# Kernel optimization log

Measured on AMD Instinct MI355X. Metric: run time of the kernel, lower is better.

The kernel has to match this reference:

```python
import jax, jax.numpy as jnp
import numpy as np

H = 128          # hidden / embed dim
NH = 4           # attention heads
HD = H // NH     # head dim = 32
MFD = 4          # missile feat dim
FOD = 15         # full obs dim
NEG_SLOPE = 0.01 # LeakyReLU default


def _gru(x_seq, h0, wih, whh, bih, bhh):
    # x_seq: [B,S,H], h0: [B,H]; torch GRU gate math
    def step(h, x):
        gi = x @ wih.T + bih            # [B,3H]
        gh = h @ whh.T + bhh
        i_r, i_z, i_n = jnp.split(gi, 3, axis=-1)
        h_r, h_z, h_n = jnp.split(gh, 3, axis=-1)
        r = jax.nn.sigmoid(i_r + h_r)
        z = jax.nn.sigmoid(i_z + h_z)
        n = jnp.tanh(i_n + r * h_n)
        h_new = (1.0 - z) * n + z * h
        return h_new, h_new
    h_last, outs = jax.lax.scan(step, h0, jnp.swapaxes(x_seq, 0, 1))
    return jnp.swapaxes(outs, 0, 1), h_last  # [B,S,H], [B,H]


def _ln(x, w, b, eps=1e-5):
    mu = jnp.mean(x, axis=-1, keepdims=True)
    var = jnp.var(x, axis=-1, keepdims=True)
    return (x - mu) * jax.lax.rsqrt(var + eps) * w + b


def setup_inputs() -> dict:
    key = jax.random.key(0)
    ks = jax.random.split(key, 24)
    B, S = 4096, 64
    s = 0.02
    p = {
        "obs": jax.random.normal(ks[0], (B, S, FOD), jnp.float32),
        "h0": jnp.zeros((1, B, H), jnp.float32),
        "enc_air_w": jax.random.normal(ks[1], (H, FOD)) * s,
        "enc_air_b": jnp.zeros((H,)),
        "enc_m_w": jax.random.normal(ks[2], (H, MFD)) * s,
        "enc_m_b": jnp.zeros((H,)),
        "gru_wih": jax.random.normal(ks[3], (3 * H, H)) * s,
        "gru_whh": jax.random.normal(ks[4], (3 * H, H)) * s,
        "gru_bih": jnp.zeros((3 * H,)),
        "gru_bhh": jnp.zeros((3 * H,)),
        "qln_w": jnp.ones((H,)), "qln_b": jnp.zeros((H,)),
        "kln_w": jnp.ones((H,)), "kln_b": jnp.zeros((H,)),
        "attn_in_w": jax.random.normal(ks[5], (3 * H, H)) * s,
        "attn_in_b": jnp.zeros((3 * H,)),
        "attn_out_w": jax.random.normal(ks[6], (H, H)) * s,
        "attn_out_b": jnp.zeros((H,)),
        "mlp0_w": jax.random.normal(ks[7], (H, H)) * s,
        "mlp0_b": jnp.zeros((H,)),
        "mlp1_w": jax.random.normal(ks[8], (H, H)) * s,
        "mlp1_b": jnp.zeros((H,)),
        "fco_w": jax.random.normal(ks[9], (1, H)) * s,
        "fco_b": jnp.zeros((1,)),
    }
    return {k: v.astype(jnp.float32) for k, v in p.items()}


def reference(obs, h0, enc_air_w, enc_air_b, enc_m_w, enc_m_b,
              gru_wih, gru_whh, gru_bih, gru_bhh,
              qln_w, qln_b, kln_w, kln_b,
              attn_in_w, attn_in_b, attn_out_w, attn_out_b,
              mlp0_w, mlp0_b, mlp1_w, mlp1_b, fco_w, fco_b):
    B, S, _ = obs.shape
    N = B * S
    # aircraft encoder + GRU with residual
    air_embed = obs @ enc_air_w.T + enc_air_b                      # [B,S,H]
    gru_out, h_last = _gru(air_embed, h0[0], gru_wih, gru_whh, gru_bih, gru_bhh)
    air_feat = (gru_out + air_embed).reshape(N, H)                 # [N,H]
    # missile encoders (shared weights, two missiles)
    m_raw = obs[..., :2 * MFD].reshape(N, 2, MFD)                  # [N,2,4]
    keys_raw = m_raw @ enc_m_w.T + enc_m_b                         # [N,2,H]
    # inactive-missile mask
    inactive = jnp.array([1.0, 0.0, 1.0, 0.0], obs.dtype)
    mask = jnp.all(jnp.isclose(m_raw, inactive, rtol=1e-5, atol=1e-8), axis=-1)  # [N,2]
    # layer norms
    q_n = _ln(air_feat[:, None, :], qln_w, qln_b)                  # [N,1,H]
    k_n = _ln(keys_raw, kln_w, kln_b)                              # [N,2,H]
    # multihead attention (1 query, 2 keys), values are raw keys
    wq, wk, wv = jnp.split(attn_in_w, 3, axis=0)
    bq, bk, bv = jnp.split(attn_in_b, 3, axis=0)
    q = (q_n @ wq.T + bq).reshape(N, 1, NH, HD)
    k = (k_n @ wk.T + bk).reshape(N, 2, NH, HD)
    v = (keys_raw @ wv.T + bv).reshape(N, 2, NH, HD)
    scores = jnp.einsum('nqhd,nkhd->nhqk', q, k) / jnp.sqrt(jnp.float32(HD))
    scores = scores + jnp.where(mask, -jnp.inf, 0.0)[:, None, None, :]
    attn = jax.nn.softmax(scores, axis=-1)                         # [N,NH,1,2]
    ctx = jnp.einsum('nhqk,nkhd->nqhd', attn, v).reshape(N, H)
    attn_out = ctx @ attn_out_w.T + attn_out_b                     # [N,H]
    attn_out = jnp.where(jnp.isnan(attn_out), 0.0, attn_out)       # nan_to_num guard
    combined = air_feat + attn_out
    # MLP head
    h1 = jax.nn.leaky_relu(combined @ mlp0_w.T + mlp0_b, NEG_SLOPE)
    h2 = jax.nn.leaky_relu(h1 @ mlp1_w.T + mlp1_b, NEG_SLOPE)
    val = h2 @ fco_w.T + fco_b                                     # [N,1]
    return val, h_last[None]
```

## Files before the change

kernel.cpp:

```cpp
#include <hip/hip_runtime.h>
#include <math.h>

#define B_   4096
#define S_   64
#define H_   128
#define N_   (B_*S_)

#define WS_WC    0
#define WS_BC    6144
#define WS_WAP   6528
#define WS_WQP   8576
#define WS_SQ    24960
#define WS_EQ    25088
#define WS_KC    25216
#define WS_EK1   25728
#define WS_SK    25856
#define WS_EK2   25984
#define WS_VC    26112
#define WS_VB    26624
#define WS_MV    26752
#define WS_QQ    26756
#define WS_QLIN  26772
#define WS_MBC   26776
#define WS_C0    26777
#define WS_PB    27392
#define WS_WO2T  (WS_PB + 5120)
#define WS_SROW  (WS_PB + 7808)
#define WS_EROW  (WS_PB + 7836)
#define WS_GB    60160
#define WS_AIR   92928
#define TOKS     64

typedef __attribute__((ext_vector_type(8))) short bf16x8;
typedef __attribute__((ext_vector_type(4))) float f32x4;

extern "C" __device__ float __ocml_native_exp2_f32(float);

__device__ __forceinline__ float dot4(float4 a, float4 b){
    return fmaf(a.x,b.x, fmaf(a.y,b.y, fmaf(a.z,b.z, a.w*b.w)));
}
__device__ __forceinline__ unsigned short f2bf(float f){
    union { float f; unsigned u; } v; v.f = f;
    unsigned r = v.u + 0x7FFF + ((v.u >> 16) & 1);
    return (unsigned short)(r >> 16);
}
__device__ __forceinline__ float bf2f(unsigned short u){
    union { unsigned u; float f; } v; v.u = ((unsigned)u) << 16;
    return v.f;
}
__device__ __forceinline__ unsigned cvtpk_bf16(float a, float b){
    unsigned r;
    asm("v_cvt_pk_bf16_f32 %0, %1, %2" : "=v"(r) : "v"(a), "v"(b));
    return r;
}

#define KL_SCALE (-1.4426950408889634f)
#define KN_SCALE ( 2.8853900817779268f)

__global__ void precompute_kernel(
    const float* __restrict__ enc_air_w, const float* __restrict__ enc_air_b,
    const float* __restrict__ enc_m_w,  const float* __restrict__ enc_m_b,
    const float* __restrict__ gru_wih,  const float* __restrict__ gru_bih,
    const float* __restrict__ qln_w, const float* __restrict__ qln_b,
    const float* __restrict__ kln_w, const float* __restrict__ kln_b,
    const float* __restrict__ attn_in_w, const float* __restrict__ attn_in_b,
    const float* __restrict__ attn_out_w,
    const float* __restrict__ mlp0_w, const float* __restrict__ mlp1_w,
    float* __restrict__ ws)
{
    int i = blockIdx.x*blockDim.x + threadIdx.x;
    if (i < 6144) {
        int o = i>>4, f = i&15; float a = 0.f;
        if (f < 15) for (int k=0;k<128;k++) a = fmaf(gru_wih[o*128+k], enc_air_w[k*15+f], a);
        ws[WS_WC+i] = a;
    } else if (i < 6528) {
        int o = i-6144; float a = gru_bih[o];
        for (int k=0;k<128;k++) a = fmaf(gru_wih[o*128+k], enc_air_b[k], a);
        ws[WS_BC+o] = a;
    } else if (i < 8576) {
        int idx = i-6528; int j = idx>>4, f = idx&15;
        ws[WS_WAP+idx] = (f<15) ? enc_air_w[j*15+f] : 0.f;
    } else if (i < 24960) {
        int idx = i-8576; int o = idx>>7, j = idx&127;
        ws[WS_WQP+idx] = attn_in_w[o*128+j]*qln_w[j];
    } else if (i < 25088) {
        int o = i-24960; float a=0.f;
        for (int j=0;j<128;j++) a = fmaf(attn_in_w[o*128+j], qln_w[j], a);
        ws[WS_SQ+o]=a;
    } else if (i < 25216) {
        int o = i-25088; float a = attn_in_b[o];
        for (int j=0;j<128;j++) a = fmaf(attn_in_w[o*128+j], qln_b[j], a);
        ws[WS_EQ+o]=a;
    } else if (i < 25728) {
        int idx = i-25216; int o = idx>>2, f = idx&3; float a=0.f;
        for (int j=0;j<128;j++) a = fmaf(attn_in_w[(128+o)*128+j]*kln_w[j], enc_m_w[j*4+f], a);
        ws[WS_KC+idx]=a;
    } else if (i < 25856) {
        int o = i-25728; float a=0.f;
        for (int j=0;j<128;j++) a = fmaf(attn_in_w[(128+o)*128+j]*kln_w[j], enc_m_b[j], a);
        ws[WS_EK1+o]=a;
    } else if (i < 25984) {
        int o = i-25856; float a=0.f;
        for (int j=0;j<128;j++) a = fmaf(attn_in_w[(128+o)*128+j], kln_w[j], a);
        ws[WS_SK+o]=a;
    } else if (i < 26112) {
        int o = i-25984; float a = attn_in_b[128+o];
        for (int j=0;j<128;j++) a = fmaf(attn_in_w[(128+o)*128+j], kln_b[j], a);
        ws[WS_EK2+o]=a;
    } else if (i < 26624) {
        int idx = i-26112; int o = idx>>2, f = idx&3; float a=0.f;
        for (int j=0;j<128;j++) a = fmaf(attn_in_w[(256+o)*128+j], enc_m_w[j*4+f], a);
        ws[WS_VC+idx]=a;
    } else if (i < 26752) {
        int o = i-26624; float a = attn_in_b[256+o];
        for (int j=0;j<128;j++) a = fmaf(attn_in_w[(256+o)*128+j], enc_m_b[j], a);
        ws[WS_VB+o]=a;
    } else if (i < 26756) {
        int f = i-26752; float a=0.f;
        for (int j=0;j<128;j++) a += enc_m_w[j*4+f];
        ws[WS_MV+f]=a*(1.f/128.f);
    } else if (i < 26772) {
        int idx = i-26756; int a4 = idx>>2, b4 = idx&3; float a=0.f;
        for (int j=0;j<128;j++) a = fmaf(enc_m_w[j*4+a4], enc_m_w[j*4+b4], a);
        ws[WS_QQ+idx]=a*(1.f/128.f);
    } else if (i < 26776) {
        int f = i-26772; float a=0.f;
        for (int j=0;j<128;j++) a = fmaf(enc_m_b[j], enc_m_w[j*4+f], a);
        ws[WS_QLIN+f]=a*(2.f/128.f);
    } else if (i == 26776) {
        float a=0.f; for (int j=0;j<128;j++) a += enc_m_b[j];
        ws[WS_MBC]=a*(1.f/128.f);
    } else if (i == 26777) {
        float a=0.f; for (int j=0;j<128;j++) a = fmaf(enc_m_b[j], enc_m_b[j], a);
        ws[WS_C0]=a*(1.f/128.f);
    } else if (i >= 32768 && i < 98304) {
        int idx = i - 32768;
        int mm = idx>>14;
        if (mm >= 2) {
            int i8 = idx & 7, l = (idx>>3)&63, p = (idx>>9)&3, wv = (idx>>11)&7;
            int n = 16*wv + (l&15);
            int k = 32*p + ((l>>4)<<3) + i8;
            float v = (mm==2) ? mlp0_w[n*128+k] : mlp1_w[n*128+k];
            ((unsigned short*)(ws+WS_PB))[idx] = f2bf(v);
        }
    }
}

__global__ void pack_gru_kernel(const float* __restrict__ whh, float* __restrict__ ws)
{
    int idx = blockIdx.x*blockDim.x + threadIdx.x;
    int i8 = idx&7, l=(idx>>3)&63, w=(idx>>9)&7, f=idx>>12;
    int n = 16*w + (l&15);
    int k = ((l>>4)<<3) + i8;
    float v = 0.f;
    if (f < 5) {
        int kk = f*32 + k;
        if (kk < 128) v = whh[n*128 + kk];
        else { int kl = kk-128; if (kl<16) v = ws[WS_WC + n*16 + kl]; }
        v *= KL_SCALE;
    } else if (f < 10) {
        int kk = (f-5)*32 + k;
        if (kk < 128) v = whh[(128+n)*128 + kk];
        else { int kl = kk-128; if (kl<16) v = ws[WS_WC + (128+n)*16 + kl]; }
        v *= KL_SCALE;
    } else if (f < 14) {
        int kk = (f-10)*32 + k;
        v = whh[(256+n)*128 + kk] * KN_SCALE;
    } else if (f == 14) {
        if (k < 16) v = ws[WS_WC + (256+n)*16 + k] * KN_SCALE;
    } else {
        if (k < 16) v = ws[WS_WAP + n*16 + k];
    }
    ((unsigned short*)(ws+WS_GB))[idx] = f2bf(v);
}

__global__ void pack2_kernel(const float* __restrict__ wo, const float* __restrict__ bo,
                             float* __restrict__ ws)
{
    int i = blockIdx.x*blockDim.x + threadIdx.x;
    if (i < 4096) {
        int i8=i&7, l=(i>>3)&63, p=(i>>9)&3, ct=(i>>11)&1;
        int r = 16*ct + (l&15);
        int k = 32*p + ((l>>4)<<3) + i8;
        float v = 0.f;
        if (r < 28){
            int h = r/7, u = r - h*7;
            float a = 0.f;
            for (int d5=0; d5<32; d5++){
                int d = h*32 + d5;
                float c = (u<4) ? ws[WS_KC + d*4 + u]
                        : (u==4) ? ws[WS_EK1 + d]
                        : (u==5) ? ws[WS_SK + d]
                        :          ws[WS_EK2 + d];
                a = fmaf(c, ws[WS_WQP + d*128 + k], a);
            }
            v = a;
        } else if (r == 31) {
            v = 1.f;
        }
        ((unsigned short*)(ws+WS_PB))[i] = f2bf(v);
    } else if (i < 4152) {
        int j = i - 4096; int r = j % 28; int era = j / 28;
        int h = r/7, u = r - h*7;
        float a = 0.f;
        for (int d5=0; d5<32; d5++){
            int d = h*32 + d5;
            float c = (u<4) ? ws[WS_KC + d*4 + u]
                    : (u==4) ? ws[WS_EK1 + d]
                    : (u==5) ? ws[WS_SK + d]
                    :          ws[WS_EK2 + d];
            a = fmaf(c, ws[(era ? WS_EQ : WS_SQ) + d], a);
        }
        ws[(era ? WS_EROW : WS_SROW) + r] = a;
    } else if (i >= 4224 && i < 6912) {
        int j = i - 4224; int c = j>>7, o = j&127;
        float a;
        if (c == 20) a = bo[o];
        else {
            int h = c/5, u = c - h*5;
            a = 0.f;
            for (int d5=0; d5<32; d5++){
                int d = h*32 + d5;
                float cv = (u<4) ? ws[WS_VC + d*4 + u] : ws[WS_VB + d];
                a = fmaf(wo[o*128 + d], cv, a);
            }
        }
        ws[WS_WO2T + c*128 + o] = a;
    }
}

__global__ void pack3_kernel(const float* __restrict__ mlp0_w,
                             const float* __restrict__ fcw,
                             float* __restrict__ ws)
{
    int i = blockIdx.x*blockDim.x + threadIdx.x;
    if (i < 4096){
        int i8=i&7, l=(i>>3)&63, w=(i>>9)&7;
        int n = 16*w + (l&15);
        int c = ((l>>4)<<3) + i8;
        float v = 0.f;
        if (c < 21){
            float a = 0.f;
            const float* wo2 = ws + WS_WO2T + c*128;
            for (int o=0;o<128;o++) a = fmaf(mlp0_w[n*128+o], wo2[o], a);
            v = a;
        }
        ((unsigned short*)(ws+WS_PB))[4096 + i] = f2bf(v);
    } else {
        int j = i - 4096;
        int i8=j&7, l=(j>>3)&63, p=(j>>9)&3;
        int k = 32*p + ((l>>4)<<3) + i8;
        float v = ((l&15)==0) ? fcw[k] : 0.f;
        ((unsigned short*)(ws+WS_PB))[8192 + j] = f2bf(v);
    }
}

__global__ __launch_bounds__(512) void gru_kernel(
    const float* __restrict__ obs, const float* __restrict__ h0,
    const float* __restrict__ bhh, const float* __restrict__ ba,
    const float* __restrict__ ws,
    unsigned short* __restrict__ air, float* __restrict__ out)
{
    __shared__ __align__(16) unsigned short Abf[2][16*136];
    __shared__ __align__(16) unsigned short obs_lds[64*16*24];
    __shared__ __align__(16) unsigned short zero16[8];

    const int t = threadIdx.x;
    const int w = t>>6;
    const int l = t&63;
    const int quad = l>>4;
    const int col  = l&15;
    const int jj   = 16*w + col;
    const int row0 = blockIdx.x*16;

    const unsigned short* gb = (const unsigned short*)(ws + WS_GB);
    bf16x8 bf[16];
    #pragma unroll
    for (int f=0; f<16; f++) bf[f] = *(const bf16x8*)&gb[(f*8 + w)*512 + l*8];

    const float bcrt = KL_SCALE*(ws[WS_BC+jj]     + bhh[jj]);
    const float bczt = KL_SCALE*(ws[WS_BC+128+jj] + bhh[128+jj]);
    const float bcn  = KN_SCALE*ws[WS_BC+256+jj];
    const float bhn  = KN_SCALE*bhh[256+jj];
    const float baj  = ba[jj];
    const f32x4 cR = {bcrt,bcrt,bcrt,bcrt};
    const f32x4 cZ = {bczt,bczt,bczt,bczt};
    const f32x4 cG = {bcn,bcn,bcn,bcn};
    const f32x4 cE = {baj,baj,baj,baj};
    const f32x4 cN = {bhn,bhn,bhn,bhn};

    float hreg[4];
    #pragma unroll
    for (int reg=0; reg<4; reg++)
        hreg[reg] = h0[(size_t)(row0+quad*4+reg)*128 + jj];

    if (t < 8) zero16[t] = 0;

    {
        int rr = t>>5, c0 = (t&31)*4;
        float4 hv = *(const float4*)&h0[(size_t)(row0+rr)*128 + c0];
        unsigned long long pk = (unsigned long long)f2bf(hv.x)
              | ((unsigned long long)f2bf(hv.y)<<16)
              | ((unsigned long long)f2bf(hv.z)<<32)
              | ((unsigned long long)f2bf(hv.w)<<48);
        *(unsigned long long*)&Abf[0][rr*136 + c0] = pk;
    }

    #pragma unroll
    for (int it=0; it<8; it++){
        int pair = it*128 + (t>>2);
        int sub  = t&3;
        int tok = pair>>6, s = pair&63;
        const float* op = &obs[((size_t)(row0+tok)*64 + s)*15 + sub*4];
        unsigned long long pk = 0;
        #pragma unroll
        for (int k=0;k<4;k++){
            int c = sub*4+k;
            float ov = (c<15) ? op[k] : 0.f;
            pk |= ((unsigned long long)f2bf(ov)) << (16*k);
        }
        *(unsigned long long*)&obs_lds[(s*16+tok)*24 + sub*4] = pk;
    }
    __syncthreads();

    unsigned short* ap0 = air + (size_t)(row0 + quad*4 + 0)*8192 + jj;
    unsigned short* ap1 = air + (size_t)(row0 + quad*4 + 1)*8192 + jj;
    unsigned short* ap2 = air + (size_t)(row0 + quad*4 + 2)*8192 + jj;
    unsigned short* ap3 = air + (size_t)(row0 + quad*4 + 3)*8192 + jj;
    const int anb = (quad*4)*136 + jj;

    f32x4 oR, oZ, oG, oE;
    {
        const unsigned short* osrc = (quad<2)
            ? &obs_lds[(0*16+col)*24 + quad*8] : &zero16[0];
        bf16x8 a4 = *(const bf16x8*)osrc;
        oR = __builtin_amdgcn_mfma_f32_16x16x32_bf16(a4, bf[4],  cR, 0,0,0);
        oZ = __builtin_amdgcn_mfma_f32_16x16x32_bf16(a4, bf[9],  cZ, 0,0,0);
        oG = __builtin_amdgcn_mfma_f32_16x16x32_bf16(a4, bf[14], cG, 0,0,0);
        oE = __builtin_amdgcn_mfma_f32_16x16x32_bf16(a4, bf[15], cE, 0,0,0);
    }

    unsigned short* const A0 = &Abf[0][0];
    unsigned short* const A1 = &Abf[1][0];

#define GRU_STEP(S, AC, AN)                                                        \
    {                                                                              \
        bf16x8 a0 = *(const bf16x8*)&(AC)[col*136 +  0 + quad*8];                  \
        bf16x8 a1 = *(const bf16x8*)&(AC)[col*136 + 32 + quad*8];                  \
        bf16x8 a2 = *(const bf16x8*)&(AC)[col*136 + 64 + quad*8];                  \
        bf16x8 a3 = *(const bf16x8*)&(AC)[col*136 + 96 + quad*8];                  \
        f32x4 aR = oR, aZ = oZ;                                                    \
        f32x4 aN = cN;                                                             \
        aR = __builtin_amdgcn_mfma_f32_16x16x32_bf16(a0, bf[0],  aR, 0,0,0);       \
        aR = __builtin_amdgcn_mfma_f32_16x16x32_bf16(a1, bf[1],  aR, 0,0,0);       \
        aR = __builtin_amdgcn_mfma_f32_16x16x32_bf16(a2, bf[2],  aR, 0,0,0);       \
        aR = __builtin_amdgcn_mfma_f32_16x16x32_bf16(a3, bf[3],  aR, 0,0,0);       \
        aZ = __builtin_amdgcn_mfma_f32_16x16x32_bf16(a0, bf[5],  aZ, 0,0,0);       \
        aZ = __builtin_amdgcn_mfma_f32_16x16x32_bf16(a1, bf[6],  aZ, 0,0,0);       \
        aZ = __builtin_amdgcn_mfma_f32_16x16x32_bf16(a2, bf[7],  aZ, 0,0,0);       \
        aZ = __builtin_amdgcn_mfma_f32_16x16x32_bf16(a3, bf[8],  aZ, 0,0,0);       \
        aN = __builtin_amdgcn_mfma_f32_16x16x32_bf16(a0, bf[10], aN, 0,0,0);       \
        aN = __builtin_amdgcn_mfma_f32_16x16x32_bf16(a1, bf[11], aN, 0,0,0);       \
        aN = __builtin_amdgcn_mfma_f32_16x16x32_bf16(a2, bf[12], aN, 0,0,0);       \
        aN = __builtin_amdgcn_mfma_f32_16x16x32_bf16(a3, bf[13], aN, 0,0,0);       \
        f32x4 nR, nZ, nG, nE;                                                      \
        if ((S) < 63){                                                             \
            const unsigned short* osrc = (quad<2)                                  \
                ? &obs_lds[(((S)+1)*16+col)*24 + quad*8] : &zero16[0];             \
            bf16x8 a4 = *(const bf16x8*)osrc;                                      \
            nR = __builtin_amdgcn_mfma_f32_16x16x32_bf16(a4, bf[4],  cR, 0,0,0);   \
            nZ = __builtin_amdgcn_mfma_f32_16x16x32_bf16(a4, bf[9],  cZ, 0,0,0);   \
            nG = __builtin_amdgcn_mfma_f32_16x16x32_bf16(a4, bf[14], cG, 0,0,0);   \
            nE = __builtin_amdgcn_mfma_f32_16x16x32_bf16(a4, bf[15], cE, 0,0,0);   \
        }                                                                          \
        float hnv[4], avv[4];                                                      \
        _Pragma("unroll")                                                          \
        for (int reg=0; reg<4; reg++){                                             \
            float rg = __builtin_amdgcn_rcpf(1.f + __ocml_native_exp2_f32(aR[reg]));\
            float zg = __builtin_amdgcn_rcpf(1.f + __ocml_native_exp2_f32(aZ[reg]));\
            float nx = fmaf(rg, aN[reg], oG[reg]);                                 \
            float e2 = __ocml_native_exp2_f32(nx);                                 \
            float ng = 1.f - 2.f*__builtin_amdgcn_rcpf(e2 + 1.f);                  \
            float hn = fmaf(zg, hreg[reg]-ng, ng);                                 \
            hreg[reg] = hn;                                                        \
            hnv[reg] = hn;                                                         \
            avv[reg] = hn + oE[reg];                                               \
        }                                                                          \
        unsigned ph01 = cvtpk_bf16(hnv[0], hnv[1]);                                \
        unsigned ph23 = cvtpk_bf16(hnv[2], hnv[3]);                                \
        unsigned pa01 = cvtpk_bf16(avv[0], avv[1]);                                \
        unsigned pa23 = cvtpk_bf16(avv[2], avv[3]);                                \
        (AN)[anb        ] = (unsigned short)ph01;                                  \
        (AN)[anb + 136  ] = (unsigned short)(ph01 >> 16);                          \
        (AN)[anb + 272  ] = (unsigned short)ph23;                                  \
        (AN)[anb + 408  ] = (unsigned short)(ph23 >> 16);                          \
        *ap0 = (unsigned short)pa01;  *ap1 = (unsigned short)(pa01 >> 16);         \
        *ap2 = (unsigned short)pa23;  *ap3 = (unsigned short)(pa23 >> 16);         \
        ap0 += 128; ap1 += 128; ap2 += 128; ap3 += 128;                            \
        if ((S) < 63){ oR = nR; oZ = nZ; oG = nG; oE = nE; }                       \
        asm volatile("s_waitcnt lgkmcnt(0)" ::: "memory");                         \
        __builtin_amdgcn_s_barrier();                                              \
        __builtin_amdgcn_sched_barrier(0);                                         \
    }

    for (int s = 0; s < 64; s += 2){
        GRU_STEP(s,   A0, A1)
        GRU_STEP(s+1, A1, A0)
    }
#undef GRU_STEP

    #pragma unroll
    for (int reg=0; reg<4; reg++)
        out[(size_t)N_ + (size_t)(row0+quad*4+reg)*128 + jj] = hreg[reg];
}

__global__ __launch_bounds__(512) void attnmlp_kernel(
    const float* __restrict__ obs,
    const float* __restrict__ ws,
    const float* __restrict__ b0, const float* __restrict__ b1,
    const float* __restrict__ fcb,
    const unsigned short* __restrict__ air, float* __restrict__ out)
{
    __shared__ __align__(16) unsigned short U_bf[TOKS*168];
    __shared__ __align__(16) unsigned short H1_bf[TOKS*136];
    __shared__ float praw[TOKS*28];
    __shared__ float obs_m[TOKS][8];
    __shared__ float sm_s[TOKS], s2_s[TOKS];
    __shared__ float kmu_s[TOKS][2], krs_s[TOKS][2];
    __shared__ int   kmask_s[TOKS][2];
    __shared__ float sero[56];

    const int t = threadIdx.x;
    const int w = t>>6;
    const int l = t&63;
    const int quad = l>>4;
    const int col  = l&15;
    const int jj   = 16*w + col;
    const int n0 = blockIdx.x*TOKS;

    const unsigned short* pb = (const unsigned short*)(ws + WS_PB);

    {
        const int tok0 = t>>3, sub = t&7;
        const unsigned short* apx = &air[(size_t)(n0+tok0)*128 + sub*16];
        uint4 x0 = *(const uint4*)apx;
        uint4 x1 = *(const uint4*)(apx+8);
        *(uint4*)&U_bf[tok0*168 + sub*16]     = x0;
        *(uint4*)&U_bf[tok0*168 + sub*16 + 8] = x1;
        if (sub < 5){
            #pragma unroll
            for (int c=0;c<4;c++) U_bf[tok0*168 + 148 + sub*4 + c] = 0;
        }
        obs_m[tok0][sub] = obs[(size_t)(n0+tok0)*15 + sub];
    }
    if (t < 128){
        int rr = t>>1, mi = t&1;
        const float* mp = &obs[(size_t)(n0+rr)*15 + mi*4];
        float m0=mp[0], m1=mp[1], m2=mp[2], m3=mp[3];
        const float tol1 = 1e-8f + 1e-5f, tol0 = 1e-8f;
        kmask_s[rr][mi] = (fabsf(m0-1.f)<=tol1)&&(fabsf(m1)<=tol0)&&
                          (fabsf(m2-1.f)<=tol1)&&(fabsf(m3)<=tol0);
        float mv[4]={m0,m1,m2,m3};
        float mu = ws[WS_MBC];
        #pragma unroll
        for (int f=0;f<4;f++) mu = fmaf(ws[WS_MV+f], mv[f], mu);
        float e2 = ws[WS_C0];
        #pragma unroll
        for (int a4=0;a4<4;a4++){
            e2 = fmaf(ws[WS_QLIN+a4], mv[a4], e2);
            #pragma unroll
            for (int b4=0;b4<4;b4++) e2 = fmaf(ws[WS_QQ+a4*4+b4]*mv[a4], mv[b4], e2);
        }
        float var = e2 - mu*mu;
        kmu_s[rr][mi]=mu; krs_s[rr][mi]=rsqrtf(var+1e-5f);
    }
    if (t < 56) sero[t] = ws[WS_SROW + t];
    __syncthreads();

    {
        const int tt = w>>1, ct = w&1;
        const int jA = ct*16 + col;
        bf16x8 afr[4];
        #pragma unroll
        for (int p=0;p<4;p++)
            afr[p] = *(const bf16x8*)&U_bf[(tt*16+col)*168 + p*32 + quad*8];
        f32x4 acc = {0.f,0.f,0.f,0.f};
        #pragma unroll
        for (int p=0;p<4;p++)
            acc = __builtin_amdgcn_mfma_f32_16x16x32_bf16(afr[p], *(const bf16x8*)&pb[((ct*4+p)*64 + l)*8], acc, 0,0,0);
        if (ct == 1){
            f32x4 accX = {0.f,0.f,0.f,0.f};
            #pragma unroll
            for (int p=0;p<4;p++)
                accX = __builtin_amdgcn_mfma_f32_16x16x32_bf16(afr[p], afr[p], accX, 0,0,0);
            if ((col>>2) == quad) s2_s[tt*16+col] = accX[col&3];
            if (col == 15){
                #pragma unroll
                for (int reg=0;reg<4;reg++) sm_s[tt*16+quad*4+reg] = acc[reg];
            }
        }
        if (jA < 28){
            #pragma unroll
            for (int reg=0;reg<4;reg++)
                praw[(tt*16+quad*4+reg)*28 + jA] = acc[reg];
        }
    }
    __syncthreads();

    if (t < TOKS*4){
        const int tok = t>>2, h = t&3;
        float mu = sm_s[tok]*(1.f/128.f);
        float var = s2_s[tok]*(1.f/128.f) - mu*mu;
        float rs = rsqrtf(var + 1e-5f);
        const float* pr = &praw[tok*28 + h*7];
        float P[7];
        #pragma unroll
        for (int u=0;u<7;u++)
            P[u] = fmaf(rs, pr[u] - mu*sero[h*7+u], sero[28 + h*7+u]);
        const float T0=P[0],T1=P[1],T2=P[2],T3=P[3],Pa=P[4],Pb=P[5],Pc=P[6];
        const float4 m0v = *(const float4*)&obs_m[tok][0];
        const float4 m1v = *(const float4*)&obs_m[tok][4];
        const float scale = 0.17677669529663687f;
        float d0 = fmaf(T0,m0v.x, fmaf(T1,m0v.y, fmaf(T2,m0v.z, fmaf(T3,m0v.w, Pa))));
        float d1 = fmaf(T0,m1v.x, fmaf(T1,m1v.y, fmaf(T2,m1v.z, fmaf(T3,m1v.w, Pa))));
        float s0 = fmaf(krs_s[tok][0], d0 - kmu_s[tok][0]*Pb, Pc) * scale;
        float s1 = fmaf(krs_s[tok][1], d1 - kmu_s[tok][1]*Pb, Pc) * scale;
        int msk0 = kmask_s[tok][0], msk1 = kmask_s[tok][1];
        float a0, a1;
        if (msk0 && msk1){
            a0=0.f; a1=0.f;
            if (h==0) U_bf[tok*168 + 148] = 0;
        } else {
            if (h==0) U_bf[tok*168 + 148] = 0x3F80;
            if (msk0)      { a0=0.f; a1=1.f; }
            else if (msk1) { a0=1.f; a1=0.f; }
            else {
                float mx = fmaxf(s0,s1);
                float e0 = __expf(s0-mx), e1 = __expf(s1-mx);
                float inv = 1.f/(e0+e1);
                a0 = e0*inv; a1 = e1*inv;
            }
        }
        int cb = tok*168 + 128 + h*5;
        U_bf[cb+0] = f2bf(fmaf(a0, m0v.x, a1*m1v.x));
        U_bf[cb+1] = f2bf(fmaf(a0, m0v.y, a1*m1v.y));
        U_bf[cb+2] = f2bf(fmaf(a0, m0v.z, a1*m1v.z));
        U_bf[cb+3] = f2bf(fmaf(a0, m0v.w, a1*m1v.w));
        U_bf[cb+4] = f2bf(a0 + a1);
    }
    __syncthreads();

    {
        bf16x8 bfr[5];
        #pragma unroll
        for (int p=0;p<4;p++) bfr[p] = *(const bf16x8*)&pb[((2*32 + w*4 + p)*64 + l)*8];
        bfr[4] = *(const bf16x8*)&pb[4096 + (w*64 + l)*8];
        f32x4 acc[4];
        #pragma unroll
        for (int tt=0;tt<4;tt++) acc[tt] = (f32x4){0.f,0.f,0.f,0.f};
        #pragma unroll
        for (int p=0;p<5;p++){
            const int ko = p*32 + quad*8;
            #pragma unroll
            for (int tt=0;tt<4;tt++){
                bf16x8 a = *(const bf16x8*)&U_bf[(tt*16+col)*168 + ko];
                acc[tt] = __builtin_amdgcn_mfma_f32_16x16x32_bf16(a, bfr[p], acc[tt], 0,0,0);
            }
        }
        const float b0j = b0[jj];
        #pragma unroll
        for (int tt=0;tt<4;tt++){
            float vv[4];
            #pragma unroll
            for (int reg=0;reg<4;reg++){
                float v = acc[tt][reg] + b0j;
                vv[reg] = (v > 0.f) ? v : 0.01f*v;
            }
            unsigned p01 = cvtpk_bf16(vv[0], vv[1]);
            unsigned p23 = cvtpk_bf16(vv[2], vv[3]);
            int base = (tt*16 + quad*4)*136 + jj;
            H1_bf[base      ] = (unsigned short)p01;
            H1_bf[base + 136] = (unsigned short)(p01 >> 16);
            H1_bf[base + 272] = (unsigned short)p23;
            H1_bf[base + 408] = (unsigned short)(p23 >> 16);
        }
    }
    __syncthreads();

    {
        bf16x8 bfr[4];
        #pragma unroll
        for (int p=0;p<4;p++) bfr[p] = *(const bf16x8*)&pb[((3*32 + w*4 + p)*64 + l)*8];
        f32x4 acc[4];
        #pragma unroll
        for (int tt=0;tt<4;tt++) acc[tt] = (f32x4){0.f,0.f,0.f,0.f};
        #pragma unroll
        for (int p=0;p<4;p++){
            const int ko = p*32 + quad*8;
            #pragma unroll
            for (int tt=0;tt<4;tt++){
                bf16x8 a = *(const bf16x8*)&H1_bf[(tt*16+col)*136 + ko];
                acc[tt] = __builtin_amdgcn_mfma_f32_16x16x32_bf16(a, bfr[p], acc[tt], 0,0,0);
            }
        }
        const float b1j = b1[jj];
        #pragma unroll
        for (int tt=0;tt<4;tt++){
            float vv[4];
            #pragma unroll
            for (int reg=0;reg<4;reg++){
                float v = acc[tt][reg] + b1j;
                vv[reg] = (v > 0.f) ? v : 0.01f*v;
            }
            unsigned p01 = cvtpk_bf16(vv[0], vv[1]);
            unsigned p23 = cvtpk_bf16(vv[2], vv[3]);
            int base = (tt*16 + quad*4)*168 + jj;
            U_bf[base      ] = (unsigned short)p01;
            U_bf[base + 168] = (unsigned short)(p01 >> 16);
            U_bf[base + 336] = (unsigned short)p23;
            U_bf[base + 504] = (unsigned short)(p23 >> 16);
        }
    }
    __syncthreads();

    if (w < 4){
        f32x4 acc = {0.f,0.f,0.f,0.f};
        #pragma unroll
        for (int p=0;p<4;p++){
            bf16x8 a = *(const bf16x8*)&U_bf[(w*16+col)*168 + p*32 + quad*8];
            bf16x8 b = *(const bf16x8*)&pb[8192 + (p*64 + l)*8];
            acc = __builtin_amdgcn_mfma_f32_16x16x32_bf16(a, b, acc, 0, 0, 0);
        }
        if (col == 0){
            float fb = fcb[0];
            #pragma unroll
            for (int reg=0;reg<4;reg++)
                out[n0 + w*16 + quad*4 + reg] = acc[reg] + fb;
        }
    }
}

extern "C" void kernel_launch(void* const* d_in, const int* in_sizes, int n_in,
                              void* d_out, int out_size, void* d_ws, size_t ws_size,
                              hipStream_t stream) {
    const float* obs       = (const float*)d_in[0];
    const float* h0        = (const float*)d_in[1];
    const float* enc_air_w = (const float*)d_in[2];
    const float* enc_air_b = (const float*)d_in[3];
    const float* enc_m_w   = (const float*)d_in[4];
    const float* enc_m_b   = (const float*)d_in[5];
    const float* gru_wih   = (const float*)d_in[6];
    const float* gru_whh   = (const float*)d_in[7];
    const float* gru_bih   = (const float*)d_in[8];
    const float* gru_bhh   = (const float*)d_in[9];
    const float* qln_w     = (const float*)d_in[10];
    const float* qln_b     = (const float*)d_in[11];
    const float* kln_w     = (const float*)d_in[12];
    const float* kln_b     = (const float*)d_in[13];
    const float* attn_in_w = (const float*)d_in[14];
    const float* attn_in_b = (const float*)d_in[15];
    const float* attn_out_w= (const float*)d_in[16];
    const float* attn_out_b= (const float*)d_in[17];
    const float* mlp0_w    = (const float*)d_in[18];
    const float* mlp0_b    = (const float*)d_in[19];
    const float* mlp1_w    = (const float*)d_in[20];
    const float* mlp1_b    = (const float*)d_in[21];
    const float* fco_w     = (const float*)d_in[22];
    const float* fco_b     = (const float*)d_in[23];
    float* out = (float*)d_out;
    float* ws  = (float*)d_ws;
    unsigned short* air = (unsigned short*)(ws + WS_AIR);

    precompute_kernel<<<dim3(384), dim3(256), 0, stream>>>(
        enc_air_w, enc_air_b, enc_m_w, enc_m_b, gru_wih, gru_bih,
        qln_w, qln_b, kln_w, kln_b, attn_in_w, attn_in_b,
        attn_out_w, mlp0_w, mlp1_w, ws);

    pack_gru_kernel<<<dim3(256), dim3(256), 0, stream>>>(gru_whh, ws);
    pack2_kernel<<<dim3(27), dim3(256), 0, stream>>>(attn_out_w, attn_out_b, ws);
    pack3_kernel<<<dim3(24), dim3(256), 0, stream>>>(mlp0_w, fco_w, ws);

    gru_kernel<<<dim3(256), dim3(512), 0, stream>>>(
        obs, h0, gru_bhh, enc_air_b, ws, air, out);

    attnmlp_kernel<<<dim3(N_/TOKS), dim3(512), 0, stream>>>(
        obs, ws, mlp0_b, mlp1_b, fco_b, air, out);
}
```

Baseline: 222.1 us.

## Split GRU MFMA accumulation chains and use hardware bf16 pack conversions

Each GRU gate's 4-deep dependent MFMA accumulation chain is split into two independent accumulators that are interleaved and summed afterwards. The goal is to shorten the MFMA dependency latency on the serial recurrence critical path. Software bf16 rounding is also replaced with v_cvt_pk_bf16_f32 in several places, and the air-output pointer increments are folded into constant offsets. The attention softmax now uses native exp2 with the log2(e) factor folded into the scale. The split chains need extra accumulator registers and a few additions per element.

```diff
diff --git a/kernel.cpp b/kernel.cpp
--- a/kernel.cpp
+++ b/kernel.cpp
@@ -36,9 +36,6 @@
 
 extern "C" __device__ float __ocml_native_exp2_f32(float);
 
-__device__ __forceinline__ float dot4(float4 a, float4 b){
-    return fmaf(a.x,b.x, fmaf(a.y,b.y, fmaf(a.z,b.z, a.w*b.w)));
-}
 __device__ __forceinline__ unsigned short f2bf(float f){
     union { float f; unsigned u; } v; v.f = f;
     unsigned r = v.u + 0x7FFF + ((v.u >> 16) & 1);
@@ -288,6 +285,7 @@
     const f32x4 cG = {bcn,bcn,bcn,bcn};
     const f32x4 cE = {baj,baj,baj,baj};
     const f32x4 cN = {bhn,bhn,bhn,bhn};
+    const f32x4 c0 = {0.f,0.f,0.f,0.f};
 
     float hreg[4];
     #pragma unroll
@@ -297,13 +295,12 @@
     if (t < 8) zero16[t] = 0;
 
     {
-        int rr = t>>5, c0 = (t&31)*4;
-        float4 hv = *(const float4*)&h0[(size_t)(row0+rr)*128 + c0];
-        unsigned long long pk = (unsigned long long)f2bf(hv.x)
-              | ((unsigned long long)f2bf(hv.y)<<16)
-              | ((unsigned long long)f2bf(hv.z)<<32)
-              | ((unsigned long long)f2bf(hv.w)<<48);
-        *(unsigned long long*)&Abf[0][rr*136 + c0] = pk;
+        int rr = t>>5, c0i = (t&31)*4;
+        float4 hv = *(const float4*)&h0[(size_t)(row0+rr)*128 + c0i];
+        unsigned lo = cvtpk_bf16(hv.x, hv.y);
+        unsigned hi = cvtpk_bf16(hv.z, hv.w);
+        unsigned long long pk = (unsigned long long)lo | ((unsigned long long)hi << 32);
+        *(unsigned long long*)&Abf[0][rr*136 + c0i] = pk;
     }
 
     #pragma unroll
@@ -312,13 +309,14 @@
         int sub  = t&3;
         int tok = pair>>6, s = pair&63;
         const float* op = &obs[((size_t)(row0+tok)*64 + s)*15 + sub*4];
-        unsigned long long pk = 0;
-        #pragma unroll
-        for (int k=0;k<4;k++){
-            int c = sub*4+k;
-            float ov = (c<15) ? op[k] : 0.f;
-            pk |= ((unsigned long long)f2bf(ov)) << (16*k);
-        }
+        float o0 = op[0];
+        float o1 = (sub*4+1<15) ? op[1] : 0.f;
+        float o2 = (sub*4+2<15) ? op[2] : 0.f;
+        float o3 = (sub*4+3<15) ? op[3] : 0.f;
+        if (sub==3){ o3 = 0.f; }
+        unsigned lo = cvtpk_bf16(o0, o1);
+        unsigned hi = cvtpk_bf16(o2, o3);
+        unsigned long long pk = (unsigned long long)lo | ((unsigned long long)hi << 32);
         *(unsigned long long*)&obs_lds[(s*16+tok)*24 + sub*4] = pk;
     }
     __syncthreads();
@@ -343,26 +341,26 @@
     unsigned short* const A0 = &Abf[0][0];
     unsigned short* const A1 = &Abf[1][0];
 
-#define GRU_STEP(S, AC, AN)                                                        \
+#define GRU_STEP(S, AC, AN, OFF)                                                   \
     {                                                                              \
         bf16x8 a0 = *(const bf16x8*)&(AC)[col*136 +  0 + quad*8];                  \
         bf16x8 a1 = *(const bf16x8*)&(AC)[col*136 + 32 + quad*8];                  \
         bf16x8 a2 = *(const bf16x8*)&(AC)[col*136 + 64 + quad*8];                  \
         bf16x8 a3 = *(const bf16x8*)&(AC)[col*136 + 96 + quad*8];                  \
-        f32x4 aR = oR, aZ = oZ;                                                    \
-        f32x4 aN = cN;                                                             \
-        aR = __builtin_amdgcn_mfma_f32_16x16x32_bf16(a0, bf[0],  aR, 0,0,0);       \
-        aR = __builtin_amdgcn_mfma_f32_16x16x32_bf16(a1, bf[1],  aR, 0,0,0);       \
-        aR = __builtin_amdgcn_mfma_f32_16x16x32_bf16(a2, bf[2],  aR, 0,0,0);       \
-        aR = __builtin_amdgcn_mfma_f32_16x16x32_bf16(a3, bf[3],  aR, 0,0,0);       \
-        aZ = __builtin_amdgcn_mfma_f32_16x16x32_bf16(a0, bf[5],  aZ, 0,0,0);       \
-        aZ = __builtin_amdgcn_mfma_f32_16x16x32_bf16(a1, bf[6],  aZ, 0,0,0);       \
-        aZ = __builtin_amdgcn_mfma_f32_16x16x32_bf16(a2, bf[7],  aZ, 0,0,0);       \
-        aZ = __builtin_amdgcn_mfma_f32_16x16x32_bf16(a3, bf[8],  aZ, 0,0,0);       \
-        aN = __builtin_amdgcn_mfma_f32_16x16x32_bf16(a0, bf[10], aN, 0,0,0);       \
-        aN = __builtin_amdgcn_mfma_f32_16x16x32_bf16(a1, bf[11], aN, 0,0,0);       \
-        aN = __builtin_amdgcn_mfma_f32_16x16x32_bf16(a2, bf[12], aN, 0,0,0);       \
-        aN = __builtin_amdgcn_mfma_f32_16x16x32_bf16(a3, bf[13], aN, 0,0,0);       \
+        f32x4 aR = oR, aZ = oZ, aN = cN;                                           \
+        f32x4 aR2 = c0, aZ2 = c0, aN2 = c0;                                        \
+        aR  = __builtin_amdgcn_mfma_f32_16x16x32_bf16(a0, bf[0],  aR,  0,0,0);     \
+        aR2 = __builtin_amdgcn_mfma_f32_16x16x32_bf16(a1, bf[1],  aR2, 0,0,0);     \
+        aN  = __builtin_amdgcn_mfma_f32_16x16x32_bf16(a0, bf[10], aN,  0,0,0);     \
+        aN2 = __builtin_amdgcn_mfma_f32_16x16x32_bf16(a1, bf[11], aN2, 0,0,0);     \
+        aR  = __builtin_amdgcn_mfma_f32_16x16x32_bf16(a2, bf[2],  aR,  0,0,0);     \
+        aR2 = __builtin_amdgcn_mfma_f32_16x16x32_bf16(a3, bf[3],  aR2, 0,0,0);     \
+        aN  = __builtin_amdgcn_mfma_f32_16x16x32_bf16(a2, bf[12], aN,  0,0,0);     \
+        aN2 = __builtin_amdgcn_mfma_f32_16x16x32_bf16(a3, bf[13], aN2, 0,0,0);     \
+        aZ  = __builtin_amdgcn_mfma_f32_16x16x32_bf16(a0, bf[5],  aZ,  0,0,0);     \
+        aZ2 = __builtin_amdgcn_mfma_f32_16x16x32_bf16(a1, bf[6],  aZ2, 0,0,0);     \
+        aZ  = __builtin_amdgcn_mfma_f32_16x16x32_bf16(a2, bf[7],  aZ,  0,0,0);     \
+        aZ2 = __builtin_amdgcn_mfma_f32_16x16x32_bf16(a3, bf[8],  aZ2, 0,0,0);     \
         f32x4 nR, nZ, nG, nE;                                                      \
         if ((S) < 63){                                                             \
             const unsigned short* osrc = (quad<2)                                  \
@@ -376,9 +374,9 @@
         float hnv[4], avv[4];                                                      \
         _Pragma("unroll")                                                          \
         for (int reg=0; reg<4; reg++){                                             \
-            float rg = __builtin_amdgcn_rcpf(1.f + __ocml_native_exp2_f32(aR[reg]));\
-            float zg = __builtin_amdgcn_rcpf(1.f + __ocml_native_exp2_f32(aZ[reg]));\
-            float nx = fmaf(rg, aN[reg], oG[reg]);                                 \
+            float rg = __builtin_amdgcn_rcpf(1.f + __ocml_native_exp2_f32(aR[reg]+aR2[reg]));\
+            float zg = __builtin_amdgcn_rcpf(1.f + __ocml_native_exp2_f32(aZ[reg]+aZ2[reg]));\
+            float nx = fmaf(rg, aN[reg]+aN2[reg], oG[reg]);                        \
             float e2 = __ocml_native_exp2_f32(nx);                                 \
             float ng = 1.f - 2.f*__builtin_amdgcn_rcpf(e2 + 1.f);                  \
             float hn = fmaf(zg, hreg[reg]-ng, ng);                                 \
@@ -394,9 +392,8 @@
         (AN)[anb + 136  ] = (unsigned short)(ph01 >> 16);                          \
         (AN)[anb + 272  ] = (unsigned short)ph23;                                  \
         (AN)[anb + 408  ] = (unsigned short)(ph23 >> 16);                          \
-        *ap0 = (unsigned short)pa01;  *ap1 = (unsigned short)(pa01 >> 16);         \
-        *ap2 = (unsigned short)pa23;  *ap3 = (unsigned short)(pa23 >> 16);         \
-        ap0 += 128; ap1 += 128; ap2 += 128; ap3 += 128;                            \
+        ap0[OFF] = (unsigned short)pa01;  ap1[OFF] = (unsigned short)(pa01 >> 16); \
+        ap2[OFF] = (unsigned short)pa23;  ap3[OFF] = (unsigned short)(pa23 >> 16); \
         if ((S) < 63){ oR = nR; oZ = nZ; oG = nG; oE = nE; }                       \
         asm volatile("s_waitcnt lgkmcnt(0)" ::: "memory");                         \
         __builtin_amdgcn_s_barrier();                                              \
@@ -404,8 +401,9 @@
     }
 
     for (int s = 0; s < 64; s += 2){
-        GRU_STEP(s,   A0, A1)
-        GRU_STEP(s+1, A1, A0)
+        GRU_STEP(s,   A0, A1, 0)
+        GRU_STEP(s+1, A1, A0, 128)
+        ap0 += 256; ap1 += 256; ap2 += 256; ap3 += 256;
     }
 #undef GRU_STEP
 
@@ -520,7 +518,7 @@
         const float T0=P[0],T1=P[1],T2=P[2],T3=P[3],Pa=P[4],Pb=P[5],Pc=P[6];
         const float4 m0v = *(const float4*)&obs_m[tok][0];
         const float4 m1v = *(const float4*)&obs_m[tok][4];
-        const float scale = 0.17677669529663687f;
+        const float scale = 0.17677669529663687f * 1.4426950408889634f;
         float d0 = fmaf(T0,m0v.x, fmaf(T1,m0v.y, fmaf(T2,m0v.z, fmaf(T3,m0v.w, Pa))));
         float d1 = fmaf(T0,m1v.x, fmaf(T1,m1v.y, fmaf(T2,m1v.z, fmaf(T3,m1v.w, Pa))));
         float s0 = fmaf(krs_s[tok][0], d0 - kmu_s[tok][0]*Pb, Pc) * scale;
@@ -536,16 +534,19 @@
             else if (msk1) { a0=1.f; a1=0.f; }
             else {
                 float mx = fmaxf(s0,s1);
-                float e0 = __expf(s0-mx), e1 = __expf(s1-mx);
+                float e0 = __ocml_native_exp2_f32(s0-mx);
+                float e1 = __ocml_native_exp2_f32(s1-mx);
                 float inv = 1.f/(e0+e1);
                 a0 = e0*inv; a1 = e1*inv;
             }
         }
         int cb = tok*168 + 128 + h*5;
-        U_bf[cb+0] = f2bf(fmaf(a0, m0v.x, a1*m1v.x));
-        U_bf[cb+1] = f2bf(fmaf(a0, m0v.y, a1*m1v.y));
-        U_bf[cb+2] = f2bf(fmaf(a0, m0v.z, a1*m1v.z));
-        U_bf[cb+3] = f2bf(fmaf(a0, m0v.w, a1*m1v.w));
+        unsigned y01 = cvtpk_bf16(fmaf(a0, m0v.x, a1*m1v.x), fmaf(a0, m0v.y, a1*m1v.y));
+        unsigned y23 = cvtpk_bf16(fmaf(a0, m0v.z, a1*m1v.z), fmaf(a0, m0v.w, a1*m1v.w));
+        U_bf[cb+0] = (unsigned short)y01;
+        U_bf[cb+1] = (unsigned short)(y01 >> 16);
+        U_bf[cb+2] = (unsigned short)y23;
+        U_bf[cb+3] = (unsigned short)(y23 >> 16);
         U_bf[cb+4] = f2bf(a0 + a1);
     }
     __syncthreads();
```

Measured after the change: 223.7 us. Within noise of the previous version (+0.7%).
